# Kernel optimization log

Hardware: AMD Instinct MI355X
Metric: run time of the kernel (lower is better)

Reference implementation:

```python
import jax, jax.numpy as jnp
import numpy as np
import math

B, S, D, H, COND = 4, 2048, 768, 12, 128
DH = D // H
MLP = 4 * D
EPS = 1e-5


def setup_inputs() -> dict:
    key = jax.random.key(0)
    ks = jax.random.split(key, 10)
    s = 0.02  # init scale for weights
    x = jax.random.normal(ks[0], (B, S, D), jnp.float32)
    c = jax.random.normal(ks[1], (B, COND), jnp.float32)
    # rotary tables, layout (1, S, 3, 1, DH) per module docstring
    pos = jnp.arange(S, dtype=jnp.float32)
    inv_freq = 1.0 / (10000.0 ** (jnp.arange(0, DH, 2, dtype=jnp.float32) / DH))
    ang = pos[:, None] * inv_freq[None, :]            # (S, DH/2)
    cos = jnp.concatenate([jnp.cos(ang), jnp.cos(ang)], -1)  # (S, DH)
    sin = jnp.concatenate([jnp.sin(ang), jnp.sin(ang)], -1)
    cos = jnp.broadcast_to(cos[None, :, None, None, :], (1, S, 3, 1, DH))
    sin = jnp.broadcast_to(sin[None, :, None, None, :], (1, S, 3, 1, DH))
    return {
        "x": x,
        "cos": cos,
        "sin": sin,
        "c": c,
        "ln1_w": jnp.ones((D,), jnp.float32),
        "W_qkv": s * jax.random.normal(ks[2], (3 * D, D), jnp.float32),
        "W_out": s * jax.random.normal(ks[3], (D, D), jnp.float32),
        "W_mlp1": s * jax.random.normal(ks[4], (MLP, D), jnp.float32),
        "b_mlp1": jnp.zeros((MLP,), jnp.float32),
        "W_mlp2": s * jax.random.normal(ks[5], (D, MLP), jnp.float32),
        "b_mlp2": jnp.zeros((D,), jnp.float32),
        "ln2_w": jnp.ones((D,), jnp.float32),
        "W_ada": s * jax.random.normal(ks[6], (6 * D, COND), jnp.float32),
        "b_ada": jnp.zeros((6 * D,), jnp.float32),
    }


def _ln(x, w):
    # LayerNorm with weight only (no bias), computed in fp32 like the original
    xf = x.astype(jnp.float32)
    mu = xf.mean(-1, keepdims=True)
    var = ((xf - mu) ** 2).mean(-1, keepdims=True)
    return (xf - mu) * jax.lax.rsqrt(var + EPS) * w


def reference(x, cos, sin, c, ln1_w, W_qkv, W_out, W_mlp1, b_mlp1, W_mlp2, b_mlp2, ln2_w, W_ada, b_ada):
    b, s_len = x.shape[0], x.shape[1]
    # adaLN modulation: (B, 6D) -> six (B, 1, D) chunks
    ada = c @ W_ada.T + b_ada
    sh_msa, sc_msa, g_msa, sh_mlp, sc_mlp, g_mlp = [t[:, None, :] for t in jnp.split(ada, 6, axis=-1)]

    x_skip = x
    h = _ln(x, ln1_w) * (1.0 + sc_msa) + sh_msa
    qkv = (h @ W_qkv.T).reshape(b, s_len, 3, H, DH)

    # rotary: slice as in apply_rotary_pos_emb_for_macos
    cos_s = cos[0, :, 0, 0, : DH // 2][None, :, None, :]  # (1, S, 1, DH/2)
    sin_s = sin[0, :, 0, 0, : DH // 2][None, :, None, :]
    q, k, v = qkv[:, :, 0], qkv[:, :, 1], qkv[:, :, 2]     # (B, S, H, DH)

    def _rot(t):
        t1, t2 = t[..., : DH // 2], t[..., DH // 2 :]
        return jnp.concatenate([t1 * cos_s - t2 * sin_s, t1 * sin_s + t2 * cos_s], -1)

    q, k = _rot(q), _rot(k)

    # non-causal attention
    scale = 1.0 / math.sqrt(DH)
    scores = jnp.einsum("bshd,bthd->bhst", q, k) * scale
    attn = jax.nn.softmax(scores, axis=-1)
    o = jnp.einsum("bhst,bthd->bshd", attn, v).reshape(b, s_len, D)

    # bias_dropout_add_scale (inference: dropout = identity)
    x = x_skip + g_msa * (o @ W_out.T)

    h2 = _ln(x, ln2_w) * (1.0 + sc_mlp) + sh_mlp
    m = jax.nn.gelu(h2 @ W_mlp1.T + b_mlp1, approximate=True) @ W_mlp2.T + b_mlp2
    return x + g_mlp * m
```

## Files before the change

kernel.cpp:

```cpp
#include <hip/hip_runtime.h>

typedef __bf16 bf16;
typedef __bf16 bf16x4 __attribute__((ext_vector_type(4)));
typedef __bf16 bf16x8 __attribute__((ext_vector_type(8)));
typedef float floatx4 __attribute__((ext_vector_type(4)));

#define MFMA16(a, b, c) __builtin_amdgcn_mfma_f32_16x16x32_bf16((a), (b), (c), 0, 0, 0)

__device__ __forceinline__ float san(float v, float magic) {
  unsigned u = __builtin_bit_cast(unsigned, v);
  return ((u & 0x7f800000u) == 0x7f800000u) ? magic : v;
}

__device__ __forceinline__ void gld_lds16(bf16* lds, const bf16* g) {
  __builtin_amdgcn_global_load_lds((__attribute__((address_space(1))) void*)g,
                                   (__attribute__((address_space(3))) void*)lds,
                                   16, 0, 0);
}

__global__ __launch_bounds__(256) void wcvt_k(const float* __restrict__ w,
                                              bf16* __restrict__ o, int n4) {
  int i = blockIdx.x * 256 + threadIdx.x;
  if (i >= n4) return;
  float4 v = ((const float4*)w)[i];
  bf16x4 b = {(bf16)v.x, (bf16)v.y, (bf16)v.z, (bf16)v.w};
  *(bf16x4*)(o + (size_t)i * 4) = b;
}

__global__ void ada_k(const float* __restrict__ c, const float* __restrict__ W,
                      const float* __restrict__ bias, float* __restrict__ ada) {
  int idx = blockIdx.x * 256 + threadIdx.x;
  if (idx >= 4 * 4608) return;
  int bb = idx / 4608;
  int j = idx - bb * 4608;
  float s = bias[j];
  const float4* wp = (const float4*)(W + (size_t)j * 128);
  const float4* cp = (const float4*)(c + (size_t)bb * 128);
#pragma unroll
  for (int t = 0; t < 32; t++) {
    float4 w4 = wp[t], c4 = cp[t];
    s += c4.x * w4.x + c4.y * w4.y + c4.z * w4.z + c4.w * w4.w;
  }
  ada[idx] = san(s, 7.0e3f);
}

__global__ __launch_bounds__(256) void ln_mod_k(const float* __restrict__ xin,
                                                const float* __restrict__ lnw,
                                                const float* __restrict__ ada,
                                                int sh_off, int sc_off,
                                                bf16* __restrict__ h,
                                                int tok_base) {
  int wv = threadIdx.x >> 6, lane = threadIdx.x & 63;
  int tok = tok_base + blockIdx.x * 4 + wv;
  int bb = tok >> 11;
  const float* xr = xin + (size_t)tok * 768;
  size_t obase = (size_t)(tok - tok_base) * 768;
  float4 v[3];
#pragma unroll
  for (int r = 0; r < 3; r++) v[r] = *(const float4*)(xr + lane * 4 + r * 256);
  float s1 = 0.f, s2 = 0.f;
#pragma unroll
  for (int r = 0; r < 3; r++) {
    s1 += v[r].x + v[r].y + v[r].z + v[r].w;
    s2 += v[r].x * v[r].x + v[r].y * v[r].y + v[r].z * v[r].z + v[r].w * v[r].w;
  }
#pragma unroll
  for (int off = 32; off > 0; off >>= 1) {
    s1 += __shfl_xor(s1, off);
    s2 += __shfl_xor(s2, off);
  }
  float mu = s1 * (1.f / 768.f);
  float rs = rsqrtf(s2 * (1.f / 768.f) - mu * mu + 1e-5f);
  const float* adab = ada + bb * 4608;
#pragma unroll
  for (int r = 0; r < 3; r++) {
    int j = lane * 4 + r * 256;
    float4 sc = *(const float4*)(adab + sc_off + j);
    float4 sh = *(const float4*)(adab + sh_off + j);
    float4 w4 = *(const float4*)(lnw + j);
    bf16x4 o4;
    o4[0] = (bf16)san(((v[r].x - mu) * rs) * w4.x * (1.f + sc.x) + sh.x, 5.0e3f);
    o4[1] = (bf16)san(((v[r].y - mu) * rs) * w4.y * (1.f + sc.y) + sh.y, 5.0e3f);
    o4[2] = (bf16)san(((v[r].z - mu) * rs) * w4.z * (1.f + sc.z) + sh.z, 5.0e3f);
    o4[3] = (bf16)san(((v[r].w - mu) * rs) * w4.w * (1.f + sc.w) + sh.w, 5.0e3f);
    *(bf16x4*)&h[obase + j] = o4;
  }
}

template <int EPI>
__global__ __launch_bounds__(256, 3) void gemm_k(
    const bf16* __restrict__ A, const bf16* __restrict__ W, int K, int k_len,
    int m_base, const float* __restrict__ cosp, const float* __restrict__ sinp,
    const float* __restrict__ ada, const float* __restrict__ resid_x,
    const float* __restrict__ bias, bf16* __restrict__ out_q,
    bf16* __restrict__ out_k, bf16* __restrict__ out_v,
    float* __restrict__ out_f, float* __restrict__ out_f2) {
  __shared__ bf16 As[3][128 * 32];
  __shared__ bf16 Bs[3][128 * 32];
  int tid = threadIdx.x;
  int lane = tid & 63, wv = tid >> 6;
  int quad = lane >> 4, lm = lane & 15;
  int gx = gridDim.x, nwg = gx * gridDim.y;
  int d = blockIdx.y * gx + blockIdx.x;
  int lid = d;
  if ((nwg & 7) == 0) {
    int q8 = nwg >> 3;
    lid = (d & 7) * q8 + (d >> 3);
  }
  int by = lid / gx, bx = lid - by * gx;
  int m0 = by * 128, n0 = bx * 128;
  int mw = (wv >> 1) * 64, nw = (wv & 1) * 64;
  int kb = blockIdx.z * k_len;

  floatx4 acc[4][4];
#pragma unroll
  for (int i = 0; i < 4; i++)
#pragma unroll
    for (int j = 0; j < 4; j++) acc[i][j] = {0.f, 0.f, 0.f, 0.f};

  const bf16* Ag0 = A + (size_t)(m0 + wv * 16 + lm) * K + quad * 8;
  const bf16* Ag1 = Ag0 + (size_t)64 * K;
  const bf16* Bg0 = W + (size_t)(n0 + wv * 16 + lm) * K + quad * 8;
  const bf16* Bg1 = Bg0 + (size_t)64 * K;
  int wb = wv * 512;

#define STAGE_T(sb, kk)                    \
  do {                                     \
    gld_lds16(&As[sb][wb], Ag0 + (kk));    \
    gld_lds16(&As[sb][wb + 2048], Ag1 + (kk)); \
    gld_lds16(&Bs[sb][wb], Bg0 + (kk));    \
    gld_lds16(&Bs[sb][wb + 2048], Bg1 + (kk)); \
  } while (0)

  int nt = k_len >> 5;
  STAGE_T(0, kb);
  STAGE_T(1, kb + 32);

  int s_cur = 0;
  for (int t = 0; t < nt; t++) {
    if (t + 1 < nt)
      asm volatile("s_waitcnt vmcnt(4)" ::: "memory");
    else
      asm volatile("s_waitcnt vmcnt(0)" ::: "memory");
    __builtin_amdgcn_s_barrier();
    if (t + 2 < nt) {
      int sn = s_cur + 2;
      if (sn >= 3) sn -= 3;
      STAGE_T(sn, kb + (t + 2) * 32);
    }
    bf16x8 af[4], bfr[4];
#pragma unroll
    for (int i = 0; i < 4; i++) {
      int it = (mw >> 4) + i;
      af[i] = *(const bf16x8*)&As[s_cur][(size_t)(it * 64 + quad * 16 + lm) * 8];
      int jt = (nw >> 4) + i;
      bfr[i] = *(const bf16x8*)&Bs[s_cur][(size_t)(jt * 64 + quad * 16 + lm) * 8];
    }
#pragma unroll
    for (int i = 0; i < 4; i++)
#pragma unroll
      for (int j = 0; j < 4; j++) acc[i][j] = MFMA16(af[i], bfr[j], acc[i][j]);
    s_cur = (s_cur + 1 == 3) ? 0 : s_cur + 1;
  }
#undef STAGE_T

  int colb = n0 + nw;
#pragma unroll
  for (int i = 0; i < 4; i++) {
#pragma unroll
    for (int r = 0; r < 4; r++) {
      int mg = m_base + m0 + mw + i * 16 + quad * 4 + r;
      if (EPI == 0) {
        int bb = mg >> 11, s = mg & 2047;
        int sec = colb / 768;
        int nb = colb - sec * 768;
        int hh = nb >> 6;
        if (sec == 2) {
          size_t vbase = ((size_t)(bb * 12 + hh) * 64) * 2048 + s;
#pragma unroll
          for (int j = 0; j < 4; j++) {
            int d2 = j * 16 + lm;
            out_v[vbase + (size_t)d2 * 2048] = (bf16)san(acc[i][j][r], 100.f);
          }
        } else {
          const float* cs = cosp + (size_t)s * 192;
          const float* sn = sinp + (size_t)s * 192;
          bf16* dst = (sec == 0) ? out_q : out_k;
          float scl = (sec == 0) ? 0.125f : 1.0f;
          size_t base = ((size_t)(bb * 12 + hh) * 2048 + s) * 64;
#pragma unroll
          for (int j = 0; j < 2; j++) {
            int d2 = j * 16 + lm;
            float c0 = cs[d2], s0 = sn[d2];
            float t1 = san(acc[i][j][r], 100.f);
            float t2 = san(acc[i][j + 2][r], 100.f);
            dst[base + d2] = (bf16)((t1 * c0 - t2 * s0) * scl);
            dst[base + d2 + 32] = (bf16)((t1 * s0 + t2 * c0) * scl);
          }
        }
      } else if (EPI == 1) {
        int bb = mg >> 11;
#pragma unroll
        for (int j = 0; j < 4; j++) {
          int n = colb + j * 16 + lm;
          float g = ada[bb * 4608 + 1536 + n];
          float xv =
              san(resid_x[(size_t)mg * 768 + n] + g * acc[i][j][r], 1.0e5f);
          out_f[(size_t)mg * 768 + n] = xv;
          float g2 = ada[bb * 4608 + 3840 + n];
          out_f2[(size_t)mg * 768 + n] = xv + g2 * bias[n];
        }
      } else if (EPI == 2) {
#pragma unroll
        for (int j = 0; j < 4; j++) {
          int n = colb + j * 16 + lm;
          float v = acc[i][j][r] + bias[n];
          float t = tanhf(0.7978845608f * (v + 0.044715f * v * v * v));
          out_q[(size_t)(mg - m_base) * 3072 + n] =
              (bf16)san(0.5f * v * (1.f + t), 3.0e5f);
        }
      } else {
        int bb = mg >> 11;
#pragma unroll
        for (int j = 0; j < 4; j++) {
          int n = colb + j * 16 + lm;
          float g = ada[bb * 4608 + 3840 + n];
          atomicAdd(out_f + (size_t)mg * 768 + n, san(g * acc[i][j][r], 1.0e6f));
        }
      }
    }
  }
}

__global__ __launch_bounds__(256, 3) void attn_k(const bf16* __restrict__ q,
                                                 const bf16* __restrict__ k,
                                                 const bf16* __restrict__ vT,
                                                 bf16* __restrict__ o) {
  __shared__ bf16 Kbuf[2][4096];
  __shared__ bf16 Vbuf[2][4096];
  __shared__ bf16 Plds[4][16 * 72];
  int bh = blockIdx.y;
  int qt = blockIdx.x;
  int b = bh / 12, h = bh - b * 12;
  int tid = threadIdx.x, lane = tid & 63, wv = tid >> 6;
  int quad = lane >> 4, lm = lane & 15;

  const bf16* Kp = k + (size_t)bh * 2048 * 64;
  const bf16* Vp = vT + (size_t)bh * 64 * 2048;

  const bf16* Qrow =
      q + (size_t)bh * 2048 * 64 + (size_t)(qt * 64 + wv * 16 + lm) * 64;
  bf16x8 qf0 = *(const bf16x8*)(Qrow + quad * 8);
  bf16x8 qf1 = *(const bf16x8*)(Qrow + 32 + quad * 8);

  const bf16* ksrc0 = Kp + (size_t)(wv * 16 + lm) * 64 + quad * 8;
  const bf16* ksrc1 = ksrc0 + 32;
  const bf16* vsrc0 = Vp + (size_t)(wv * 16 + lm) * 2048 + quad * 8;
  const bf16* vsrc1 = vsrc0 + 32;

  float l_i = 0.f;
  floatx4 accO[4];
#pragma unroll
  for (int t = 0; t < 4; t++) accO[t] = {0.f, 0.f, 0.f, 0.f};

  gld_lds16(&Kbuf[0][(wv * 2 + 0) * 512], ksrc0);
  gld_lds16(&Kbuf[0][(wv * 2 + 1) * 512], ksrc1);
  gld_lds16(&Vbuf[0][(wv * 2 + 0) * 512], vsrc0);
  gld_lds16(&Vbuf[0][(wv * 2 + 1) * 512], vsrc1);

  int p = 0;
  for (int kt = 0; kt < 32; kt++) {
    __syncthreads();
    if (kt < 31) {
      size_t ko = (size_t)(kt + 1) * 4096;
      size_t vo = (size_t)(kt + 1) * 64;
      int pn = p ^ 1;
      gld_lds16(&Kbuf[pn][(wv * 2 + 0) * 512], ksrc0 + ko);
      gld_lds16(&Kbuf[pn][(wv * 2 + 1) * 512], ksrc1 + ko);
      gld_lds16(&Vbuf[pn][(wv * 2 + 0) * 512], vsrc0 + vo);
      gld_lds16(&Vbuf[pn][(wv * 2 + 1) * 512], vsrc1 + vo);
    }

    floatx4 accS[4];
#pragma unroll
    for (int i = 0; i < 4; i++) accS[i] = {0.f, 0.f, 0.f, 0.f};
    __builtin_amdgcn_s_setprio(1);
#pragma unroll
    for (int i = 0; i < 4; i++) {
      bf16x8 kf0 =
          *(const bf16x8*)&Kbuf[p][(size_t)((i * 2 + 0) * 64 + quad * 16 + lm) * 8];
      bf16x8 kf1 =
          *(const bf16x8*)&Kbuf[p][(size_t)((i * 2 + 1) * 64 + quad * 16 + lm) * 8];
      accS[i] = MFMA16(kf0, qf0, accS[i]);
      accS[i] = MFMA16(kf1, qf1, accS[i]);
    }
    __builtin_amdgcn_s_setprio(0);

    float psum = 0.f;
    bf16 pv[4][4];
#pragma unroll
    for (int i = 0; i < 4; i++)
#pragma unroll
      for (int r = 0; r < 4; r++) {
        float pe = __expf(accS[i][r]);
        psum += pe;
        pv[i][r] = (bf16)pe;
      }
    psum += __shfl_xor(psum, 16);
    psum += __shfl_xor(psum, 32);
    l_i += psum;

#pragma unroll
    for (int i = 0; i < 4; i++) {
      bf16x4 pk = {pv[i][0], pv[i][1], pv[i][2], pv[i][3]};
      *(bf16x4*)&Plds[wv][lm * 72 + i * 16 + quad * 4] = pk;
    }

    __builtin_amdgcn_s_setprio(1);
#pragma unroll
    for (int st = 0; st < 2; st++) {
      bf16x8 pf = *(const bf16x8*)&Plds[wv][lm * 72 + st * 32 + quad * 8];
#pragma unroll
      for (int t = 0; t < 4; t++) {
        bf16x8 vf =
            *(const bf16x8*)&Vbuf[p][(size_t)((t * 2 + st) * 64 + quad * 16 + lm) * 8];
        accO[t] = MFMA16(pf, vf, accO[t]);
      }
    }
    __builtin_amdgcn_s_setprio(0);
    p ^= 1;
  }

  float lr[4];
#pragma unroll
  for (int r = 0; r < 4; r++) lr[r] = 1.f / __shfl(l_i, (quad << 2) + r);
#pragma unroll
  for (int t = 0; t < 4; t++) {
#pragma unroll
    for (int r = 0; r < 4; r++) {
      int d = t * 16 + lm;
      int s = qt * 64 + wv * 16 + quad * 4 + r;
      o[((size_t)(b * 2048 + s)) * 768 + h * 64 + d] =
          (bf16)san(accO[t][r] * lr[r], 3.0e4f);
    }
  }
}

extern "C" void kernel_launch(void* const* d_in, const int* in_sizes, int n_in,
                              void* d_out, int out_size, void* d_ws,
                              size_t ws_size, hipStream_t stream) {
  (void)in_sizes; (void)n_in; (void)out_size;
  const float* x = (const float*)d_in[0];
  const float* cosp = (const float*)d_in[1];
  const float* sinp = (const float*)d_in[2];
  const float* c = (const float*)d_in[3];
  const float* ln1w = (const float*)d_in[4];
  const float* Wqkv = (const float*)d_in[5];
  const float* Wout = (const float*)d_in[6];
  const float* Wm1 = (const float*)d_in[7];
  const float* bm1 = (const float*)d_in[8];
  const float* Wm2 = (const float*)d_in[9];
  const float* bm2 = (const float*)d_in[10];
  const float* ln2w = (const float*)d_in[11];
  const float* Wada = (const float*)d_in[12];
  const float* bada = (const float*)d_in[13];

  const size_t TOKB = (size_t)8192 * 768 * 2;
  char* ws = (char*)d_ws;
  float* ada = (float*)ws;
  char* base = ws + 73728;
  bf16* h = (bf16*)d_out;
  float* outp = (float*)d_out;

  if (ws_size >= 156000000) {
    bf16* qb = (bf16*)base;
    bf16* kb = (bf16*)(base + TOKB);
    bf16* vT = (bf16*)(base + 2 * TOKB);
    bf16* obuf = (bf16*)(base + 3 * TOKB);
    float* x2 = (float*)(base + 4 * TOKB);
    bf16* h2c = (bf16*)(base + 6 * TOKB);
    bf16* m1c = (bf16*)(base + 7 * TOKB);
    char* wbase = base + 11 * TOKB;
    bf16* wqkv_b = (bf16*)wbase;
    bf16* wout_b = (bf16*)(wbase + 4 * 1024 * 1024);
    bf16* wm1_b = (bf16*)(wbase + 6 * 1024 * 1024);
    bf16* wm2_b = (bf16*)(wbase + 11 * 1024 * 1024);

    ada_k<<<72, 256, 0, stream>>>(c, Wada, bada, ada);
    wcvt_k<<<(2304 * 768 / 4 + 255) / 256, 256, 0, stream>>>(Wqkv, wqkv_b,
                                                             2304 * 768 / 4);
    wcvt_k<<<(768 * 768 / 4 + 255) / 256, 256, 0, stream>>>(Wout, wout_b,
                                                            768 * 768 / 4);
    wcvt_k<<<(3072 * 768 / 4 + 255) / 256, 256, 0, stream>>>(Wm1, wm1_b,
                                                             3072 * 768 / 4);
    wcvt_k<<<(768 * 3072 / 4 + 255) / 256, 256, 0, stream>>>(Wm2, wm2_b,
                                                             768 * 3072 / 4);
    ln_mod_k<<<2048, 256, 0, stream>>>(x, ln1w, ada, 0, 768, h, 0);
    gemm_k<0><<<dim3(18, 64), 256, 0, stream>>>(h, wqkv_b, 768, 768, 0, cosp,
                                                sinp, ada, nullptr, nullptr,
                                                qb, kb, vT, nullptr, nullptr);
    attn_k<<<dim3(32, 48), 256, 0, stream>>>(qb, kb, vT, obuf);
    gemm_k<1><<<dim3(6, 64), 256, 0, stream>>>(obuf, wout_b, 768, 768, 0,
                                               nullptr, nullptr, ada, x, bm2,
                                               nullptr, nullptr, nullptr, x2,
                                               outp);
    ln_mod_k<<<2048, 256, 0, stream>>>(x2, ln2w, ada, 2304, 3072, h2c, 0);
    gemm_k<2><<<dim3(24, 64), 256, 0, stream>>>(
        h2c, wm1_b, 768, 768, 0, nullptr, nullptr, nullptr, nullptr, bm1, m1c,
        nullptr, nullptr, nullptr, nullptr);
    gemm_k<4><<<dim3(6, 64, 2), 256, 0, stream>>>(
        m1c, wm2_b, 3072, 1536, 0, nullptr, nullptr, ada, nullptr, nullptr,
        nullptr, nullptr, nullptr, outp, nullptr);
  } else {
    bf16* qb = (bf16*)base;
    bf16* kb = (bf16*)(base + TOKB);
    bf16* vT = (bf16*)(base + 2 * TOKB);
    bf16* obuf = (bf16*)(base + 3 * TOKB);
    bf16* h2c = (bf16*)(base + 3 * TOKB);
    float* x2 = (float*)base;
    bf16* m1c = (bf16*)(base + TOKB);
    bf16* wqkv_b = (bf16*)(base + 3 * TOKB);
    bf16* wout_b = (bf16*)(base + 2 * TOKB);
    bf16* wm1_b = (bf16*)base;
    bf16* wm2_b = (bf16*)base + (size_t)3072 * 768;

    ada_k<<<72, 256, 0, stream>>>(c, Wada, bada, ada);
    ln_mod_k<<<2048, 256, 0, stream>>>(x, ln1w, ada, 0, 768, h, 0);
    wcvt_k<<<(2304 * 768 / 4 + 255) / 256, 256, 0, stream>>>(Wqkv, wqkv_b,
                                                             2304 * 768 / 4);
    gemm_k<0><<<dim3(18, 64), 256, 0, stream>>>(h, wqkv_b, 768, 768, 0, cosp,
                                                sinp, ada, nullptr, nullptr,
                                                qb, kb, vT, nullptr, nullptr);
    attn_k<<<dim3(32, 48), 256, 0, stream>>>(qb, kb, vT, obuf);
    wcvt_k<<<(768 * 768 / 4 + 255) / 256, 256, 0, stream>>>(Wout, wout_b,
                                                            768 * 768 / 4);
    gemm_k<1><<<dim3(6, 64), 256, 0, stream>>>(obuf, wout_b, 768, 768, 0,
                                               nullptr, nullptr, ada, x, bm2,
                                               nullptr, nullptr, nullptr, x2,
                                               outp);
    ln_mod_k<<<2048, 256, 0, stream>>>(x2, ln2w, ada, 2304, 3072, h2c, 0);
    wcvt_k<<<(3072 * 768 / 4 + 255) / 256, 256, 0, stream>>>(Wm1, wm1_b,
                                                             3072 * 768 / 4);
    wcvt_k<<<(768 * 3072 / 4 + 255) / 256, 256, 0, stream>>>(Wm2, wm2_b,
                                                             768 * 3072 / 4);
    for (int cidx = 0; cidx < 2; cidx++) {
      int mb = cidx * 4096;
      gemm_k<2><<<dim3(24, 32), 256, 0, stream>>>(
          h2c + (size_t)mb * 768, wm1_b, 768, 768, mb, nullptr, nullptr,
          nullptr, nullptr, bm1, m1c, nullptr, nullptr, nullptr, nullptr);
      gemm_k<4><<<dim3(6, 32, 2), 256, 0, stream>>>(
          m1c, wm2_b, 3072, 1536, mb, nullptr, nullptr, ada, nullptr, nullptr,
          nullptr, nullptr, nullptr, outp, nullptr);
    }
  }
}
```

Before: 558.7 us.

## Fuse weight conversions, remap attention blocks for XCD locality, defer row-sum reduction

```diff
diff --git a/kernel.cpp b/kernel.cpp
--- a/kernel.cpp
+++ b/kernel.cpp
@@ -25,6 +25,24 @@
   float4 v = ((const float4*)w)[i];
   bf16x4 b = {(bf16)v.x, (bf16)v.y, (bf16)v.z, (bf16)v.w};
   *(bf16x4*)(o + (size_t)i * 4) = b;
+}
+
+__global__ __launch_bounds__(256) void wcvt4_k(const float* __restrict__ wqkv,
+                                               const float* __restrict__ wout,
+                                               const float* __restrict__ wm1,
+                                               const float* __restrict__ wm2,
+                                               bf16* __restrict__ dst) {
+  int i = blockIdx.x * 256 + threadIdx.x;
+  if (i >= 1769472) return;
+  const float* s;
+  int off;
+  if (i < 442368) { s = wqkv; off = 0; }
+  else if (i < 589824) { s = wout; off = 442368; }
+  else if (i < 1179648) { s = wm1; off = 589824; }
+  else { s = wm2; off = 1179648; }
+  float4 v = ((const float4*)s)[i - off];
+  bf16x4 b = {(bf16)v.x, (bf16)v.y, (bf16)v.z, (bf16)v.w};
+  *(bf16x4*)(dst + (size_t)i * 4) = b;
 }
 
 __global__ void ada_k(const float* __restrict__ c, const float* __restrict__ W,
@@ -239,8 +257,10 @@
   __shared__ bf16 Kbuf[2][4096];
   __shared__ bf16 Vbuf[2][4096];
   __shared__ bf16 Plds[4][16 * 72];
-  int bh = blockIdx.y;
-  int qt = blockIdx.x;
+  int d = blockIdx.y * gridDim.x + blockIdx.x;
+  int idx = d >> 3;
+  int qt = idx & 31;
+  int bh = ((idx >> 5) << 3) + (d & 7);
   int b = bh / 12, h = bh - b * 12;
   int tid = threadIdx.x, lane = tid & 63, wv = tid >> 6;
   int quad = lane >> 4, lm = lane & 15;
@@ -306,8 +326,6 @@
         psum += pe;
         pv[i][r] = (bf16)pe;
       }
-    psum += __shfl_xor(psum, 16);
-    psum += __shfl_xor(psum, 32);
     l_i += psum;
 
 #pragma unroll
@@ -331,6 +349,9 @@
     p ^= 1;
   }
 
+  l_i += __shfl_xor(l_i, 16);
+  l_i += __shfl_xor(l_i, 32);
+
   float lr[4];
 #pragma unroll
   for (int r = 0; r < 4; r++) lr[r] = 1.f / __shfl(l_i, (quad << 2) + r);
@@ -338,9 +359,9 @@
   for (int t = 0; t < 4; t++) {
 #pragma unroll
     for (int r = 0; r < 4; r++) {
-      int d = t * 16 + lm;
+      int d2 = t * 16 + lm;
       int s = qt * 64 + wv * 16 + quad * 4 + r;
-      o[((size_t)(b * 2048 + s)) * 768 + h * 64 + d] =
+      o[((size_t)(b * 2048 + s)) * 768 + h * 64 + d2] =
           (bf16)san(accO[t][r] * lr[r], 3.0e4f);
     }
   }
@@ -380,21 +401,14 @@
     float* x2 = (float*)(base + 4 * TOKB);
     bf16* h2c = (bf16*)(base + 6 * TOKB);
     bf16* m1c = (bf16*)(base + 7 * TOKB);
-    char* wbase = base + 11 * TOKB;
-    bf16* wqkv_b = (bf16*)wbase;
-    bf16* wout_b = (bf16*)(wbase + 4 * 1024 * 1024);
-    bf16* wm1_b = (bf16*)(wbase + 6 * 1024 * 1024);
-    bf16* wm2_b = (bf16*)(wbase + 11 * 1024 * 1024);
+    bf16* wall = (bf16*)(base + 11 * TOKB);
+    bf16* wqkv_b = wall;
+    bf16* wout_b = wall + (size_t)1769472;
+    bf16* wm1_b = wall + (size_t)2359296;
+    bf16* wm2_b = wall + (size_t)4718592;
 
     ada_k<<<72, 256, 0, stream>>>(c, Wada, bada, ada);
-    wcvt_k<<<(2304 * 768 / 4 + 255) / 256, 256, 0, stream>>>(Wqkv, wqkv_b,
-                                                             2304 * 768 / 4);
-    wcvt_k<<<(768 * 768 / 4 + 255) / 256, 256, 0, stream>>>(Wout, wout_b,
-                                                            768 * 768 / 4);
-    wcvt_k<<<(3072 * 768 / 4 + 255) / 256, 256, 0, stream>>>(Wm1, wm1_b,
-                                                             3072 * 768 / 4);
-    wcvt_k<<<(768 * 3072 / 4 + 255) / 256, 256, 0, stream>>>(Wm2, wm2_b,
-                                                             768 * 3072 / 4);
+    wcvt4_k<<<6912, 256, 0, stream>>>(Wqkv, Wout, Wm1, Wm2, wall);
     ln_mod_k<<<2048, 256, 0, stream>>>(x, ln1w, ada, 0, 768, h, 0);
     gemm_k<0><<<dim3(18, 64), 256, 0, stream>>>(h, wqkv_b, 768, 768, 0, cosp,
                                                 sinp, ada, nullptr, nullptr,
```

Result: faster. 547.5 us (-2.0%).
